# Performance work log

Hardware: AMD Instinct MI355X
Metric: run time of the kernel (lower is better)

Reference implementation:

```python
import jax, jax.numpy as jnp
import numpy as np

NUM_HEADS = 16
HEAD_DIM = 64  # d_model // num_heads = 1024 // 16
NUM_BUCKETS = 20


def setup_inputs() -> dict:
    key = jax.random.key(0)
    ks = jax.random.split(key, 5)
    B, S, D = 2, 2048, 1024
    v = jax.random.normal(ks[0], (B, S, D), dtype=jnp.float32)
    k = jax.random.normal(ks[1], (B, S, D), dtype=jnp.float32)
    q = jax.random.normal(ks[2], (B, S, D), dtype=jnp.float32)
    mask = jax.random.randint(ks[3], (B, S, S), 0, 2).astype(jnp.bool_)
    diff_matrix = jax.random.randint(ks[4], (B, S, S), 0, NUM_BUCKETS)
    rel_bias = jax.random.normal(jax.random.fold_in(key, 7), (NUM_BUCKETS, NUM_HEADS), dtype=jnp.float32)
    return {"v": v, "k": k, "q": q, "mask": mask, "diff_matrix": diff_matrix, "rel_bias": rel_bias}


def _split_heads(x):
    B, S, _ = x.shape
    return x.reshape(B, S, NUM_HEADS, HEAD_DIM).transpose(0, 2, 1, 3)  # [B,H,S,hd]


def reference(v, k, q, mask, diff_matrix, rel_bias):
    B, S, D = q.shape
    qh, kh, vh = _split_heads(q), _split_heads(k), _split_heads(v)
    scale = 1.0 / jnp.sqrt(jnp.float32(HEAD_DIM))
    scores = jnp.einsum('bhqd,bhkd->bhqk', qh, kh) * scale  # [B,H,S,S]
    # relative bias: gather [B,S,S,H] -> [B,H,S,S]
    bias = rel_bias[diff_matrix].transpose(0, 3, 1, 2)
    att = jax.nn.silu(scores + bias)
    att = jnp.where(mask[:, None, :, :], att, 0.0)
    av = jnp.einsum('bhqk,bhkd->bhqd', att, vh)  # [B,H,S,hd]
    return av.transpose(0, 2, 1, 3).reshape(B, S, D)
```

## Files before the change

kernel.cpp:

```cpp
#include <hip/hip_runtime.h>
#include <hip/hip_fp16.h>
#include <cstdint>
#include <cstddef>

#define SEQ 2048
#define DM 1024
#define NH 16
#define NB 20

typedef _Float16 half8 __attribute__((ext_vector_type(8)));
typedef _Float16 half4 __attribute__((ext_vector_type(4)));
typedef _Float16 h2v __attribute__((ext_vector_type(2)));
typedef float f32x4 __attribute__((ext_vector_type(4)));
typedef float f32x2 __attribute__((ext_vector_type(2)));
typedef int i32x4 __attribute__((ext_vector_type(4)));
typedef unsigned int u32;
typedef unsigned int u32x2 __attribute__((ext_vector_type(2)));

#define KF_HALVES 4194304
#define VF_HALVES 4194304

__global__ __launch_bounds__(256) void pa_prep(
    const float* __restrict__ v, const float* __restrict__ k,
    const int* __restrict__ diff, const int* __restrict__ mask,
    _Float16* __restrict__ KF, _Float16* __restrict__ VF,
    unsigned char* __restrict__ PB) {
  const int bid = blockIdx.x, tid = threadIdx.x;
  if (bid < 2048) {
    int img = bid >> 4;
    int bb = img >> 6, kt = img & 63;
    int tix = ((bid & 15) << 8) | tid;
    int r = tix >> 7;
    int c0 = (tix & 127) << 3;
    const float* src = k + ((size_t)(bb * SEQ + kt * 32 + r)) * DM + c0;
    f32x4 a = *(const f32x4*)src;
    f32x4 c = *(const f32x4*)(src + 4);
    half8 o = {(_Float16)a[0], (_Float16)a[1], (_Float16)a[2], (_Float16)a[3],
               (_Float16)c[0], (_Float16)c[1], (_Float16)c[2], (_Float16)c[3]};
    int h = c0 >> 6, dh = (c0 >> 5) & 1, g4 = (c0 >> 3) & 3;
    int k2 = r >> 4, l16 = r & 15;
    int lane = g4 * 16 + l16;
    size_t off = ((size_t)((bb * 16 + h) * 64 + kt)) * 2048 + (k2 * 2 + dh) * 512 + lane * 8;
    *(half8*)(KF + off) = o;
  } else if (bid < 3072) {
    int b3 = bid - 2048;
    int img = b3 >> 3;
    int bb = img >> 6, kt = img & 63;
    int tix = ((b3 & 7) << 8) | tid;
    int kq = tix >> 8;
    int k2 = kq >> 2, g4 = kq & 3;
    int d0 = (tix & 255) << 2;
    const float* src = v + ((size_t)(bb * SEQ + kt * 32 + k2 * 16 + g4 * 4)) * DM + d0;
    f32x4 m0 = *(const f32x4*)(src);
    f32x4 m1 = *(const f32x4*)(src + DM);
    f32x4 m2 = *(const f32x4*)(src + 2 * DM);
    f32x4 m3 = *(const f32x4*)(src + 3 * DM);
#pragma unroll
    for (int i = 0; i < 4; ++i) {
      int d = d0 + i;
      int l16 = d & 15, dt = (d >> 4) & 3, h = d >> 6;
      int lane = g4 * 16 + l16;
      half4 o = {(_Float16)m0[i], (_Float16)m1[i], (_Float16)m2[i], (_Float16)m3[i]};
      size_t off = ((size_t)((bb * 16 + h) * 64 + kt)) * 2048 + dt * 512 + lane * 8 + k2 * 4;
      *(half4*)(VF + off) = o;
    }
  } else {
    int b4 = bid - 3072;
    int job = b4 >> 5;
    int bb = job >> 6, qblk = job & 63;
    int tix = ((b4 & 31) << 8) | tid;
    int kt = tix >> 7;
    int rem = tix & 127;
    int g4 = rem & 3, l16 = (rem >> 2) & 15, qs = rem >> 6;
    int lane = g4 * 16 + l16;
    int qrow = qblk * 32 + qs * 16 + l16;
    size_t rowbase = ((size_t)(bb * SEQ + qrow)) * SEQ;
    u32x2 wds;
#pragma unroll
    for (int k2 = 0; k2 < 2; ++k2) {
      int kk = kt * 32 + k2 * 16 + g4 * 4;
      i32x4 dv = *(const i32x4*)(diff + rowbase + kk);
      i32x4 mv = *(const i32x4*)(mask + rowbase + kk);
      u32 bk[4];
#pragma unroll
      for (int r = 0; r < 4; ++r) bk[r] = mv[r] ? (u32)dv[r] : 20u;
      u32 pi01 = bk[0] * 21 + bk[1];
      u32 pi23 = bk[2] * 21 + bk[3];
      wds[k2] = pi01 | (pi23 << 16);
    }
    size_t off = ((size_t)job) * 65536 + (size_t)kt * 1024 + (size_t)lane * 16 + (size_t)qs * 8;
    *(u32x2*)(PB + off) = wds;
  }
}

__device__ __forceinline__ void gll16(const _Float16* g, _Float16* l) {
  __builtin_amdgcn_global_load_lds(
      (const __attribute__((address_space(1))) unsigned int*)g,
      (__attribute__((address_space(3))) unsigned int*)l, 16, 0, 0);
}

__device__ __forceinline__ half4 silu4nb(const f32x4& s) {
  h2v x01 = __builtin_bit_cast(h2v, __builtin_amdgcn_cvt_pkrtz(s[0], s[1]));
  h2v x23 = __builtin_bit_cast(h2v, __builtin_amdgcn_cvt_pkrtz(s[2], s[3]));
  const h2v NL2E = {(_Float16)-1.44269504f, (_Float16)-1.44269504f};
  const h2v ONE = {(_Float16)1.0f, (_Float16)1.0f};
  h2v m01 = x01 * NL2E, m23 = x23 * NL2E;
  h2v e01 = __builtin_bit_cast(h2v, h2exp2(__builtin_bit_cast(__half2, m01)));
  h2v e23 = __builtin_bit_cast(h2v, h2exp2(__builtin_bit_cast(__half2, m23)));
  h2v d01 = e01 + ONE, d23 = e23 + ONE;
  h2v y01 = x01 * __builtin_bit_cast(h2v, h2rcp(__builtin_bit_cast(__half2, d01)));
  h2v y23 = x23 * __builtin_bit_cast(h2v, h2rcp(__builtin_bit_cast(__half2, d23)));
  return (half4){y01[0], y01[1], y23[0], y23[1]};
}

struct BiasSet { f32x4 b[2][2]; };

__global__ __launch_bounds__(256, 4) void pa_main(
    const _Float16* __restrict__ KF, const _Float16* __restrict__ VF,
    const unsigned char* __restrict__ PB, const float* __restrict__ q,
    const float* __restrict__ relbias, float* __restrict__ out) {
  __shared__ _Float16 ldsK[2][2048];
  __shared__ _Float16 ldsV[2][2048];
  __shared__ f32x2 tabF[441];

  const int tid = threadIdx.x, lane = tid & 63, wid = tid >> 6;
  const int l16 = lane & 15, g4 = lane >> 4;
  const int xcd = blockIdx.x & 7;
  const int i = blockIdx.x >> 3;
  const int b = xcd >> 2;
  const int hg = xcd & 3;
  const int h = hg * 4 + (i & 3);
  const int qgrp = i >> 2;
  const int qblk = qgrp * 4 + wid;
  const int qbase = qblk * 32;

  for (int e = tid; e < 441; e += 256) {
    int bi = e / 21, bj = e - bi * 21;
    float vi = (bi < NB) ? relbias[bi * NH + h] : -30000.0f;
    float vj = (bj < NB) ? relbias[bj * NH + h] : -30000.0f;
    tabF[e] = (f32x2){vi, vj};
  }

  half8 qf[2][2];
#pragma unroll
  for (int qs = 0; qs < 2; ++qs)
#pragma unroll
    for (int dh = 0; dh < 2; ++dh) {
      const float* s = q + ((size_t)(b * SEQ + qbase + qs * 16 + l16)) * DM + h * 64 + dh * 32 + g4 * 8;
      f32x4 a = *(const f32x4*)s;
      f32x4 c = *(const f32x4*)(s + 4);
      qf[qs][dh] = {(_Float16)(a[0] * 0.125f), (_Float16)(a[1] * 0.125f),
                    (_Float16)(a[2] * 0.125f), (_Float16)(a[3] * 0.125f),
                    (_Float16)(c[0] * 0.125f), (_Float16)(c[1] * 0.125f),
                    (_Float16)(c[2] * 0.125f), (_Float16)(c[3] * 0.125f)};
    }

  f32x4 acc[2][4];
#pragma unroll
  for (int qs = 0; qs < 2; ++qs)
#pragma unroll
    for (int dt = 0; dt < 4; ++dt) acc[qs][dt] = (f32x4){0.f, 0.f, 0.f, 0.f};

  const _Float16* kfb = KF + ((size_t)((b * 16 + h) * 64)) * 2048 + lane * 8;
  const _Float16* vfb = VF + ((size_t)((b * 16 + h) * 64)) * 2048 + lane * 8;
  const unsigned char* pbb = PB + ((size_t)(b * 64 + qblk)) * 65536 + lane * 16;
  const int c512 = wid * 512;

#define STAGE(T, B)                                          \
  do {                                                       \
    gll16(kfb + (size_t)(T) * 2048 + c512, &ldsK[B][c512]);  \
    gll16(vfb + (size_t)(T) * 2048 + c512, &ldsV[B][c512]);  \
  } while (0)
#define CLMP(T) ((T) < 64 ? (T) : 63)

#define GATHER(BS, PQ)                                                 \
  do {                                                                 \
    _Pragma("unroll") for (int qs = 0; qs < 2; ++qs)                   \
      _Pragma("unroll") for (int k2 = 0; k2 < 2; ++k2) {               \
        u32 w = (u32)PQ[qs * 2 + k2];                                  \
        f32x2 p01 = tabF[w & 0xffffu];                                 \
        f32x2 p23 = tabF[w >> 16];                                     \
        BS.b[qs][k2] = (f32x4){p01[0], p01[1], p23[0], p23[1]};        \
      }                                                                \
  } while (0)

#define COMPUTE(B, BS)                                                                       \
  do {                                                                                       \
    half8 kfr[4], vvr[4];                                                                    \
    _Pragma("unroll") for (int j = 0; j < 4; ++j) {                                          \
      kfr[j] = *(const half8*)&ldsK[B][j * 512 + lane * 8];                                  \
      vvr[j] = *(const half8*)&ldsV[B][j * 512 + lane * 8];                                  \
    }                                                                                        \
    f32x4 sa[2][2];                                                                          \
    _Pragma("unroll") for (int qs = 0; qs < 2; ++qs)                                         \
      _Pragma("unroll") for (int k2 = 0; k2 < 2; ++k2) {                                     \
        sa[qs][k2] = __builtin_amdgcn_mfma_f32_16x16x32_f16(kfr[k2 * 2 + 0], qf[qs][0],      \
                                                            BS.b[qs][k2], 0, 0, 0);          \
        sa[qs][k2] = __builtin_amdgcn_mfma_f32_16x16x32_f16(kfr[k2 * 2 + 1], qf[qs][1],      \
                                                            sa[qs][k2], 0, 0, 0);            \
      }                                                                                      \
    half8 pf8[2];                                                                            \
    _Pragma("unroll") for (int qs = 0; qs < 2; ++qs) {                                       \
      half4 p0 = silu4nb(sa[qs][0]);                                                         \
      half4 p1 = silu4nb(sa[qs][1]);                                                         \
      pf8[qs] = (half8){p0[0], p0[1], p0[2], p0[3], p1[0], p1[1], p1[2], p1[3]};             \
    }                                                                                        \
    _Pragma("unroll") for (int qs = 0; qs < 2; ++qs)                                         \
      _Pragma("unroll") for (int dt = 0; dt < 4; ++dt)                                       \
        acc[qs][dt] = __builtin_amdgcn_mfma_f32_16x16x32_f16(pf8[qs], vvr[dt],               \
                                                             acc[qs][dt], 0, 0, 0);          \
  } while (0)

  BiasSet biasA, biasB;
  i32x4 pq1, pqX;

  STAGE(0, 0);
  i32x4 pq0 = *(const i32x4*)(pbb);
  pq1 = *(const i32x4*)(pbb + 1024);
  __syncthreads();
  GATHER(biasA, pq0);

  for (int t = 0; t < 64; t += 2) {
    STAGE(t + 1, 1);
    pqX = *(const i32x4*)(pbb + (size_t)CLMP(t + 2) * 1024);
    __builtin_amdgcn_sched_barrier(0);
    GATHER(biasB, pq1);
    COMPUTE(0, biasA);
    __syncthreads();
    STAGE(CLMP(t + 2), 0);
    pq1 = *(const i32x4*)(pbb + (size_t)CLMP(t + 3) * 1024);
    __builtin_amdgcn_sched_barrier(0);
    GATHER(biasA, pqX);
    COMPUTE(1, biasB);
    __syncthreads();
  }
#undef STAGE
#undef CLMP
#undef GATHER
#undef COMPUTE

#pragma unroll
  for (int qs = 0; qs < 2; ++qs)
#pragma unroll
    for (int dt = 0; dt < 4; ++dt)
#pragma unroll
      for (int r = 0; r < 4; ++r) {
        int qrow = qbase + qs * 16 + g4 * 4 + r;
        int d = h * 64 + dt * 16 + l16;
        out[((size_t)(b * SEQ) + qrow) * DM + d] = acc[qs][dt][r];
      }
}

extern "C" void kernel_launch(void* const* d_in, const int* in_sizes, int n_in,
                              void* d_out, int out_size, void* d_ws, size_t ws_size,
                              hipStream_t stream) {
  const float* v = (const float*)d_in[0];
  const float* k = (const float*)d_in[1];
  const float* q = (const float*)d_in[2];
  const int* mask = (const int*)d_in[3];
  const int* diff = (const int*)d_in[4];
  const float* relbias = (const float*)d_in[5];
  float* out = (float*)d_out;

  _Float16* KF = (_Float16*)d_ws;
  _Float16* VF = KF + KF_HALVES;
  unsigned char* PB = (unsigned char*)(VF + VF_HALVES);
  if (ws_size < (size_t)25165824) return;

  pa_prep<<<7168, 256, 0, stream>>>(v, k, diff, mask, KF, VF, PB);
  pa_main<<<512, 256, 0, stream>>>(KF, VF, PB, q, relbias, out);
}
```

Before: 91.44 us.

## Use 4-slot LDS ring with two tiles per barrier and fp16 bias add

Replaces the double-buffered K/V LDS staging with a 4-slot ring, so two tiles are prefetched while two are computed and only one barrier is needed per pair of tiles. The bias table is stored as packed fp16 pairs and the bias is added in fp16 before SiLU, instead of being fed as the fp32 MFMA accumulator input. This halves barrier count and shrinks bias gather traffic, at the cost of more LDS (32KB ring) and extra packed adds, plus slightly lower precision for the bias sum.

```diff
diff --git a/kernel.cpp b/kernel.cpp
--- a/kernel.cpp
+++ b/kernel.cpp
@@ -12,7 +12,6 @@
 typedef _Float16 half4 __attribute__((ext_vector_type(4)));
 typedef _Float16 h2v __attribute__((ext_vector_type(2)));
 typedef float f32x4 __attribute__((ext_vector_type(4)));
-typedef float f32x2 __attribute__((ext_vector_type(2)));
 typedef int i32x4 __attribute__((ext_vector_type(4)));
 typedef unsigned int u32;
 typedef unsigned int u32x2 __attribute__((ext_vector_type(2)));
@@ -99,9 +98,9 @@
       (__attribute__((address_space(3))) unsigned int*)l, 16, 0, 0);
 }
 
-__device__ __forceinline__ half4 silu4nb(const f32x4& s) {
-  h2v x01 = __builtin_bit_cast(h2v, __builtin_amdgcn_cvt_pkrtz(s[0], s[1]));
-  h2v x23 = __builtin_bit_cast(h2v, __builtin_amdgcn_cvt_pkrtz(s[2], s[3]));
+__device__ __forceinline__ half4 silu4b(const f32x4& s, h2v b01, h2v b23) {
+  h2v x01 = __builtin_bit_cast(h2v, __builtin_amdgcn_cvt_pkrtz(s[0], s[1])) + b01;
+  h2v x23 = __builtin_bit_cast(h2v, __builtin_amdgcn_cvt_pkrtz(s[2], s[3])) + b23;
   const h2v NL2E = {(_Float16)-1.44269504f, (_Float16)-1.44269504f};
   const h2v ONE = {(_Float16)1.0f, (_Float16)1.0f};
   h2v m01 = x01 * NL2E, m23 = x23 * NL2E;
@@ -113,15 +112,14 @@
   return (half4){y01[0], y01[1], y23[0], y23[1]};
 }
 
-struct BiasSet { f32x4 b[2][2]; };
+struct BiasSet { h2v b[2][2][2]; };
 
 __global__ __launch_bounds__(256, 4) void pa_main(
     const _Float16* __restrict__ KF, const _Float16* __restrict__ VF,
     const unsigned char* __restrict__ PB, const float* __restrict__ q,
     const float* __restrict__ relbias, float* __restrict__ out) {
-  __shared__ _Float16 ldsK[2][2048];
-  __shared__ _Float16 ldsV[2][2048];
-  __shared__ f32x2 tabF[441];
+  __shared__ _Float16 ring[4][4096];
+  __shared__ u32 tabH[441];
 
   const int tid = threadIdx.x, lane = tid & 63, wid = tid >> 6;
   const int l16 = lane & 15, g4 = lane >> 4;
@@ -138,7 +136,7 @@
     int bi = e / 21, bj = e - bi * 21;
     float vi = (bi < NB) ? relbias[bi * NH + h] : -30000.0f;
     float vj = (bj < NB) ? relbias[bj * NH + h] : -30000.0f;
-    tabF[e] = (f32x2){vi, vj};
+    tabH[e] = __builtin_bit_cast(u32, __builtin_amdgcn_cvt_pkrtz(vi, vj));
   }
 
   half8 qf[2][2];
@@ -166,43 +164,44 @@
   const unsigned char* pbb = PB + ((size_t)(b * 64 + qblk)) * 65536 + lane * 16;
   const int c512 = wid * 512;
 
-#define STAGE(T, B)                                          \
-  do {                                                       \
-    gll16(kfb + (size_t)(T) * 2048 + c512, &ldsK[B][c512]);  \
-    gll16(vfb + (size_t)(T) * 2048 + c512, &ldsV[B][c512]);  \
+#define STAGE(T)                                                            \
+  do {                                                                      \
+    int sl_ = (T) & 3;                                                      \
+    gll16(kfb + (size_t)(T) * 2048 + c512, &ring[sl_][c512]);               \
+    gll16(vfb + (size_t)(T) * 2048 + c512, &ring[sl_][2048 + c512]);        \
   } while (0)
 #define CLMP(T) ((T) < 64 ? (T) : 63)
 
-#define GATHER(BS, PQ)                                                 \
-  do {                                                                 \
-    _Pragma("unroll") for (int qs = 0; qs < 2; ++qs)                   \
-      _Pragma("unroll") for (int k2 = 0; k2 < 2; ++k2) {               \
-        u32 w = (u32)PQ[qs * 2 + k2];                                  \
-        f32x2 p01 = tabF[w & 0xffffu];                                 \
-        f32x2 p23 = tabF[w >> 16];                                     \
-        BS.b[qs][k2] = (f32x4){p01[0], p01[1], p23[0], p23[1]};        \
-      }                                                                \
+#define GATHER(BS, PQ)                                                      \
+  do {                                                                      \
+    _Pragma("unroll") for (int qs = 0; qs < 2; ++qs)                        \
+      _Pragma("unroll") for (int k2 = 0; k2 < 2; ++k2) {                    \
+        u32 w = (u32)PQ[qs * 2 + k2];                                       \
+        BS.b[qs][k2][0] = __builtin_bit_cast(h2v, tabH[w & 0xffffu]);       \
+        BS.b[qs][k2][1] = __builtin_bit_cast(h2v, tabH[w >> 16]);           \
+      }                                                                     \
   } while (0)
 
-#define COMPUTE(B, BS)                                                                       \
+#define COMPUTE(SL, BS)                                                                      \
   do {                                                                                       \
+    const f32x4 zf = {0.f, 0.f, 0.f, 0.f};                                                   \
     half8 kfr[4], vvr[4];                                                                    \
     _Pragma("unroll") for (int j = 0; j < 4; ++j) {                                          \
-      kfr[j] = *(const half8*)&ldsK[B][j * 512 + lane * 8];                                  \
-      vvr[j] = *(const half8*)&ldsV[B][j * 512 + lane * 8];                                  \
+      kfr[j] = *(const half8*)&ring[SL][j * 512 + lane * 8];                                 \
+      vvr[j] = *(const half8*)&ring[SL][2048 + j * 512 + lane * 8];                          \
     }                                                                                        \
     f32x4 sa[2][2];                                                                          \
     _Pragma("unroll") for (int qs = 0; qs < 2; ++qs)                                         \
       _Pragma("unroll") for (int k2 = 0; k2 < 2; ++k2) {                                     \
         sa[qs][k2] = __builtin_amdgcn_mfma_f32_16x16x32_f16(kfr[k2 * 2 + 0], qf[qs][0],      \
-                                                            BS.b[qs][k2], 0, 0, 0);          \
+                                                            zf, 0, 0, 0);                    \
         sa[qs][k2] = __builtin_amdgcn_mfma_f32_16x16x32_f16(kfr[k2 * 2 + 1], qf[qs][1],      \
                                                             sa[qs][k2], 0, 0, 0);            \
       }                                                                                      \
     half8 pf8[2];                                                                            \
     _Pragma("unroll") for (int qs = 0; qs < 2; ++qs) {                                       \
-      half4 p0 = silu4nb(sa[qs][0]);                                                         \
-      half4 p1 = silu4nb(sa[qs][1]);                                                         \
+      half4 p0 = silu4b(sa[qs][0], BS.b[qs][0][0], BS.b[qs][0][1]);                          \
+      half4 p1 = silu4b(sa[qs][1], BS.b[qs][1][0], BS.b[qs][1][1]);                          \
       pf8[qs] = (half8){p0[0], p0[1], p0[2], p0[3], p1[0], p1[1], p1[2], p1[3]};             \
     }                                                                                        \
     _Pragma("unroll") for (int qs = 0; qs < 2; ++qs)                                         \
@@ -211,28 +210,28 @@
                                                              acc[qs][dt], 0, 0, 0);          \
   } while (0)
 
-  BiasSet biasA, biasB;
-  i32x4 pq1, pqX;
-
-  STAGE(0, 0);
-  i32x4 pq0 = *(const i32x4*)(pbb);
-  pq1 = *(const i32x4*)(pbb + 1024);
+  BiasSet bE, bO;
+  i32x4 pqE, pqO, pqE2, pqO2;
+
+  STAGE(0);
+  STAGE(1);
+  pqE = *(const i32x4*)(pbb);
+  pqO = *(const i32x4*)(pbb + 1024);
   __syncthreads();
-  GATHER(biasA, pq0);
 
   for (int t = 0; t < 64; t += 2) {
-    STAGE(t + 1, 1);
-    pqX = *(const i32x4*)(pbb + (size_t)CLMP(t + 2) * 1024);
+    STAGE(CLMP(t + 2));
+    STAGE(CLMP(t + 3));
+    pqE2 = *(const i32x4*)(pbb + (size_t)CLMP(t + 2) * 1024);
+    pqO2 = *(const i32x4*)(pbb + (size_t)CLMP(t + 3) * 1024);
     __builtin_amdgcn_sched_barrier(0);
-    GATHER(biasB, pq1);
-    COMPUTE(0, biasA);
+    GATHER(bE, pqE);
+    GATHER(bO, pqO);
+    COMPUTE(t & 3, bE);
+    COMPUTE((t + 1) & 3, bO);
     __syncthreads();
-    STAGE(CLMP(t + 2), 0);
-    pq1 = *(const i32x4*)(pbb + (size_t)CLMP(t + 3) * 1024);
-    __builtin_amdgcn_sched_barrier(0);
-    GATHER(biasA, pqX);
-    COMPUTE(1, biasB);
-    __syncthreads();
+    pqE = pqE2;
+    pqO = pqO2;
   }
 #undef STAGE
 #undef CLMP
```

Result: slower. 93.89 us (+2.7%).
